# Performance work log

Measured on AMD Instinct MI355X. Metric: run time of the kernel, lower is better.

Reference implementation:

```python
import jax, jax.numpy as jnp
import numpy as np

KS = 3          # kernel_size
PAD = 1         # padding
STRIDE = 1      # stride
INC = 32
OUTC = 64
N = KS * KS     # number of sampling points


def conv2d(x, w, b, stride, pad):
    out = jax.lax.conv_general_dilated(
        x, w, (stride, stride), [(pad, pad), (pad, pad)],
        dimension_numbers=('NCHW', 'OIHW', 'NCHW'))
    return out if b is None else out + b[None, :, None, None]


def setup_inputs() -> dict:
    key = jax.random.key(0)
    k = jax.random.split(key, 5)
    x = jax.random.normal(k[0], (2, INC, 192, 192), jnp.float32)
    # main conv: kernel=ks, stride=ks, bias=None in the original
    conv_w = jax.random.normal(k[1], (OUTC, INC, KS, KS), jnp.float32) * (1.0 / np.sqrt(INC * KS * KS))
    # p_conv: weight init to 0 in the original (output = bias broadcast); unused in the math
    p_conv_w = jnp.zeros((2 * N, INC, 3, 3), jnp.float32)
    p_conv_b = jax.random.uniform(k[2], (2 * N,), jnp.float32, minval=-0.05, maxval=0.05)
    # p_conv1: produces scalar scale map A; keep it near 1 for realistic sampling
    p1_w = jax.random.normal(k[3], (1, INC, 3, 3), jnp.float32) * 0.05
    p1_b = jax.random.uniform(k[4], (1,), jnp.float32, minval=0.9, maxval=1.1)
    return {'x': x, 'conv_w': conv_w, 'p_conv_w': p_conv_w, 'p_conv_b': p_conv_b,
            'p1_w': p1_w, 'p1_b': p1_b}


def _gather_xq(xp, qx, qy, Wp):
    # xp: (b,c,Hp,Wp); qx,qy: (b,h,w,N) int -> (b,c,h,w,N)
    b, c = xp.shape[0], xp.shape[1]
    xf = xp.reshape(b, c, -1)
    idx = qx * Wp + qy  # linear index into flattened padded map (matches torch gather)
    def per_b(xf_b, idx_b):
        return xf_b[:, idx_b.ravel()].reshape((c,) + idx_b.shape)
    return jax.vmap(per_b)(xf, idx)


def _forward(x, conv_w, p_conv_w, p_conv_b, p1_w, p1_b):
    dt = x.dtype
    offset = conv2d(x, p_conv_w, p_conv_b, STRIDE, 1)   # (b,2N,h,w) -- shape-only in original
    A = conv2d(x, p1_w, p1_b, STRIDE, 1)                # (b,1,h,w) scale map
    h, w = offset.shape[2], offset.shape[3]
    xp = jnp.pad(x, ((0, 0), (0, 0), (PAD, PAD), (PAD, PAD)))
    Hp, Wp = xp.shape[2], xp.shape[3]

    # p_n: kernel-relative grid offsets, shape (1,2N,1,1)
    rng = jnp.arange(-(KS - 1) // 2, (KS - 1) // 2 + 1)
    pnx, pny = jnp.meshgrid(rng, rng, indexing='ij')
    p_n = jnp.concatenate([pnx.ravel(), pny.ravel()]).astype(dt).reshape(1, 2 * N, 1, 1)
    # p_0: absolute center coords starting at 1 (accounts for zero padding)
    gx, gy = jnp.meshgrid(jnp.arange(1, h * STRIDE + 1, STRIDE),
                          jnp.arange(1, w * STRIDE + 1, STRIDE), indexing='ij')
    p_0 = jnp.concatenate([jnp.tile(gx[None], (N, 1, 1)),
                           jnp.tile(gy[None], (N, 1, 1))], 0)[None].astype(dt)

    p = p_0 + A * p_n                       # (b,2N,h,w): scaled sampling grid
    p = jnp.transpose(p, (0, 2, 3, 1))      # (b,h,w,2N)

    q_lt = jnp.floor(p)
    q_rb = q_lt + 1
    qx_lt = jnp.clip(q_lt[..., :N], 0, Hp - 1).astype(jnp.int32)
    qy_lt = jnp.clip(q_lt[..., N:], 0, Wp - 1).astype(jnp.int32)
    qx_rb = jnp.clip(q_rb[..., :N], 0, Hp - 1).astype(jnp.int32)
    qy_rb = jnp.clip(q_rb[..., N:], 0, Wp - 1).astype(jnp.int32)

    px = jnp.clip(p[..., :N], 0, Hp - 1)
    py = jnp.clip(p[..., N:], 0, Wp - 1)

    fx_lt, fy_lt = qx_lt.astype(dt), qy_lt.astype(dt)
    fx_rb, fy_rb = qx_rb.astype(dt), qy_rb.astype(dt)
    g_lt = (1 + (fx_lt - px)) * (1 + (fy_lt - py))
    g_rb = (1 - (fx_rb - px)) * (1 - (fy_rb - py))
    g_lb = (1 + (fx_lt - px)) * (1 - (fy_rb - py))   # q_lb = (x_lt, y_rb)
    g_rt = (1 - (fx_rb - px)) * (1 + (fy_lt - py))   # q_rt = (x_rb, y_lt)

    x_lt = _gather_xq(xp, qx_lt, qy_lt, Wp)
    x_rb = _gather_xq(xp, qx_rb, qy_rb, Wp)
    x_lb = _gather_xq(xp, qx_lt, qy_rb, Wp)
    x_rt = _gather_xq(xp, qx_rb, qy_lt, Wp)

    # bilinear combine -> (b,c,h,w,N)
    x_offset = (g_lt[:, None] * x_lt + g_rb[:, None] * x_rb
                + g_lb[:, None] * x_lb + g_rt[:, None] * x_rt)

    # the ks-stride conv over the reshaped [h*ks, w*ks] map is exactly a
    # contraction over (c, n) with n = ki*ks + kj (same ordering as p_n flatten)
    wk = conv_w.reshape(conv_w.shape[0], conv_w.shape[1], N)
    out = jnp.einsum('ocn,bchwn->bohw', wk, x_offset)
    return out


def reference(x, conv_w, p_conv_w, p_conv_b, p1_w, p1_b):
    return _forward(x, conv_w, p_conv_w, p_conv_b, p1_w, p1_b)
```

## Files before the change

kernel.cpp:

```cpp
#include <hip/hip_runtime.h>

typedef __attribute__((ext_vector_type(4))) float f32x4;
typedef __attribute__((ext_vector_type(4))) int   i32x4;
typedef __attribute__((ext_vector_type(8))) short s16x8;

__device__ __forceinline__ unsigned short f2bf_rn(float f) {
  union { float f; unsigned u; } v; v.f = f;
  unsigned r = v.u + 0x7fffu + ((v.u >> 16) & 1u);
  return (unsigned short)(r >> 16);
}

__device__ __forceinline__ int packbf2(float lo, float hi) {
  union { float f; unsigned u; } a, b; a.f = lo; b.f = hi;
  return (int)__builtin_amdgcn_perm(b.u + 0x8000u, a.u + 0x8000u, 0x07060302u);
}

__device__ __forceinline__ void add8(i32x4 v, float g, f32x4& s0, f32x4& s1) {
  union { int ii; float ff; } u;
  u.ii = v[0] << 16;                  s0[0] = fmaf(g, u.ff, s0[0]);
  u.ii = v[0] & (int)0xffff0000u;     s0[1] = fmaf(g, u.ff, s0[1]);
  u.ii = v[1] << 16;                  s0[2] = fmaf(g, u.ff, s0[2]);
  u.ii = v[1] & (int)0xffff0000u;     s0[3] = fmaf(g, u.ff, s0[3]);
  u.ii = v[2] << 16;                  s1[0] = fmaf(g, u.ff, s1[0]);
  u.ii = v[2] & (int)0xffff0000u;     s1[1] = fmaf(g, u.ff, s1[1]);
  u.ii = v[3] << 16;                  s1[2] = fmaf(g, u.ff, s1[2]);
  u.ii = v[3] & (int)0xffff0000u;     s1[3] = fmaf(g, u.ff, s1[3]);
}

__device__ __forceinline__ void axis_cw(float p, int& il, int& ir, float& gl, float& gr) {
  float fl = floorf(p);
  float ql = fminf(fmaxf(fl, 0.f), 193.f);
  float qr = fminf(fmaxf(fl + 1.f, 0.f), 193.f);
  float pc = fminf(fmaxf(p, 0.f), 193.f);
  gl = 1.f + (ql - pc);
  gr = 1.f - (qr - pc);
  il = (int)ql; ir = (int)qr;
}

__global__ __launch_bounds__(256) void k_prep(const float* __restrict__ x,
                                              unsigned short* __restrict__ xp,
                                              const float* __restrict__ w,
                                              short* __restrict__ wf) {
  int t = blockIdx.x * 256 + threadIdx.x;
  if (t < 2 * 194 * 194 * 4) {
    int pix = t >> 2, c8 = t & 3;
    int b = pix / (194 * 194);
    int r = pix % (194 * 194);
    int i = r / 194 - 1, j = r % 194 - 1;
    bool ok = ((unsigned)i < 192u) && ((unsigned)j < 192u);
    const float* src = x + (size_t)b * 32 * 36864 + (size_t)(c8 * 8) * 36864 + i * 192 + j;
    unsigned v[8];
    #pragma unroll
    for (int k = 0; k < 8; k++) v[k] = ok ? (unsigned)f2bf_rn(src[k * 36864]) : 0u;
    i32x4 pv;
    pv[0] = (int)(v[0] | (v[1] << 16));
    pv[1] = (int)(v[2] | (v[3] << 16));
    pv[2] = (int)(v[4] | (v[5] << 16));
    pv[3] = (int)(v[6] | (v[7] << 16));
    *(i32x4*)(xp + (size_t)pix * 32 + c8 * 8) = pv;
  } else {
    int u = t - 2 * 194 * 194 * 4;
    if (u >= 9 * 4 * 64) return;
    int n = u / 256;
    int ot = (u / 64) % 4;
    int lane = u % 64;
    int o = ot * 16 + (lane & 15);
    int cb = (lane >> 4) * 8;
    #pragma unroll
    for (int jj = 0; jj < 8; jj++) {
      float v = w[(o * 32 + cb + jj) * 9 + n];
      wf[(size_t)u * 8 + jj] = (short)f2bf_rn(v);
    }
  }
}

__global__ __launch_bounds__(256) void k_main(const unsigned short* __restrict__ xp,
                                              const float* __restrict__ p1w,
                                              const float* __restrict__ p1b,
                                              const s16x8* __restrict__ wfv,
                                              float* __restrict__ out) {
  __shared__ float wlds[288];
  for (int idx = threadIdx.x; idx < 288; idx += 256) {
    int c = idx / 9, tap = idx % 9;
    wlds[tap * 32 + c] = p1w[idx];
  }
  __syncthreads();

  int lane = threadIdx.x & 63;
  int bs = (blockIdx.x & 7) * 144 + (blockIdx.x >> 3);
  int W = bs * 4 + (threadIdx.x >> 6);
  int b = W / 2304;
  int r = W % 2304;
  int i = r / 12;
  int j0 = (r % 12) * 16;
  int m = lane & 15, quad = lane >> 4;
  int j = j0 + m;
  const unsigned short* xpb = xp + (size_t)b * (194 * 194 * 32) + quad * 8;

  float a = 0.f;
  i32x4 vcen;
  #pragma unroll
  for (int tap = 0; tap < 9; tap++) {
    int kh = tap / 3, kw = tap % 3;
    i32x4 v = *(const i32x4*)(xpb + ((i + kh) * 194 + (j + kw)) * 32);
    if (tap == 4) vcen = v;
    const f32x4* wp = (const f32x4*)(wlds + tap * 32 + quad * 8);
    f32x4 w0 = wp[0], w1 = wp[1];
    union { int ii; float ff; } u;
    u.ii = v[0] << 16;              a = fmaf(u.ff, w0[0], a);
    u.ii = v[0] & (int)0xffff0000u; a = fmaf(u.ff, w0[1], a);
    u.ii = v[1] << 16;              a = fmaf(u.ff, w0[2], a);
    u.ii = v[1] & (int)0xffff0000u; a = fmaf(u.ff, w0[3], a);
    u.ii = v[2] << 16;              a = fmaf(u.ff, w1[0], a);
    u.ii = v[2] & (int)0xffff0000u; a = fmaf(u.ff, w1[1], a);
    u.ii = v[3] << 16;              a = fmaf(u.ff, w1[2], a);
    u.ii = v[3] & (int)0xffff0000u; a = fmaf(u.ff, w1[3], a);
  }
  a += __shfl_xor(a, 16);
  a += __shfl_xor(a, 32);
  float A = a + p1b[0];

  float cx = (float)(i + 1), cy = (float)(j + 1);
  int icx = i + 1, icy = j + 1;
  int offs[9][4];
  float gws[9][4];
  #pragma unroll
  for (int n = 0; n < 9; n++) {
    const int dx = n / 3 - 1, dy = n % 3 - 1;
    if (dx == 0 && dy == 0) continue;
    if (dy == 0) {
      int il, ir; float gl, gr;
      axis_cw(cx + A * (float)dx, il, ir, gl, gr);
      offs[n][0] = (il * 194 + icy) * 32; gws[n][0] = gl;
      offs[n][1] = (ir * 194 + icy) * 32; gws[n][1] = gr;
    } else if (dx == 0) {
      int il, ir; float gl, gr;
      axis_cw(cy + A * (float)dy, il, ir, gl, gr);
      offs[n][0] = (icx * 194 + il) * 32; gws[n][0] = gl;
      offs[n][1] = (icx * 194 + ir) * 32; gws[n][1] = gr;
    } else {
      int ilx, irx, ily, iry; float gxl, gxr, gyl, gyr;
      axis_cw(cx + A * (float)dx, ilx, irx, gxl, gxr);
      axis_cw(cy + A * (float)dy, ily, iry, gyl, gyr);
      offs[n][0] = (ilx * 194 + ily) * 32; gws[n][0] = gxl * gyl;
      offs[n][1] = (irx * 194 + iry) * 32; gws[n][1] = gxr * gyr;
      offs[n][2] = (ilx * 194 + iry) * 32; gws[n][2] = gxl * gyr;
      offs[n][3] = (irx * 194 + ily) * 32; gws[n][3] = gxr * gyl;
    }
  }

  const int cnt[9] = {4, 2, 4, 2, 0, 2, 4, 2, 4};
  i32x4 dat[9][4];
  f32x4 acc0 = {0.f, 0.f, 0.f, 0.f};
  f32x4 acc1 = acc0, acc2 = acc0, acc3 = acc0;

#define LOAD_STEP(n)                                                      \
  { _Pragma("unroll") for (int c = 0; c < 4; c++)                         \
      if (c < cnt[n]) dat[n][c] = *(const i32x4*)(xpb + offs[n][c]); }

#define PROC_STEP(n)                                                      \
  { f32x4 s0 = {0.f, 0.f, 0.f, 0.f}, s1 = s0;                             \
    _Pragma("unroll") for (int c = 0; c < 4; c++)                         \
      if (c < cnt[n]) add8(dat[n][c], gws[n][c], s0, s1);                 \
    s16x8 af; int* ai = (int*)&af;                                        \
    ai[0] = packbf2(s0[0], s0[1]); ai[1] = packbf2(s0[2], s0[3]);         \
    ai[2] = packbf2(s1[0], s1[1]); ai[3] = packbf2(s1[2], s1[3]);         \
    int wb = (n) * 256 + lane;                                            \
    acc0 = __builtin_amdgcn_mfma_f32_16x16x32_bf16(af, wfv[wb],       acc0, 0, 0, 0); \
    acc1 = __builtin_amdgcn_mfma_f32_16x16x32_bf16(af, wfv[wb + 64],  acc1, 0, 0, 0); \
    acc2 = __builtin_amdgcn_mfma_f32_16x16x32_bf16(af, wfv[wb + 128], acc2, 0, 0, 0); \
    acc3 = __builtin_amdgcn_mfma_f32_16x16x32_bf16(af, wfv[wb + 192], acc3, 0, 0, 0); }

  LOAD_STEP(0) LOAD_STEP(1) LOAD_STEP(2)
  LOAD_STEP(3) LOAD_STEP(5)
  PROC_STEP(0) PROC_STEP(1) PROC_STEP(2)
  LOAD_STEP(6) LOAD_STEP(7) LOAD_STEP(8)
  {
    s16x8 af; int* ai = (int*)&af;
    ai[0] = vcen[0]; ai[1] = vcen[1]; ai[2] = vcen[2]; ai[3] = vcen[3];
    int wb = 4 * 256 + lane;
    acc0 = __builtin_amdgcn_mfma_f32_16x16x32_bf16(af, wfv[wb],       acc0, 0, 0, 0);
    acc1 = __builtin_amdgcn_mfma_f32_16x16x32_bf16(af, wfv[wb + 64],  acc1, 0, 0, 0);
    acc2 = __builtin_amdgcn_mfma_f32_16x16x32_bf16(af, wfv[wb + 128], acc2, 0, 0, 0);
    acc3 = __builtin_amdgcn_mfma_f32_16x16x32_bf16(af, wfv[wb + 192], acc3, 0, 0, 0);
  }
  PROC_STEP(3) PROC_STEP(5)
  PROC_STEP(6) PROC_STEP(7) PROC_STEP(8)
#undef LOAD_STEP
#undef PROC_STEP

  int o0 = lane & 15;
  int jout = j0 + quad * 4;
  float* op = out + (size_t)b * 64 * 36864 + (size_t)o0 * 36864 + i * 192 + jout;
  *(f32x4*)(op) = acc0;
  *(f32x4*)(op + 16 * 36864) = acc1;
  *(f32x4*)(op + 32 * 36864) = acc2;
  *(f32x4*)(op + 48 * 36864) = acc3;
}

extern "C" void kernel_launch(void* const* d_in, const int* in_sizes, int n_in,
                              void* d_out, int out_size, void* d_ws, size_t ws_size,
                              hipStream_t stream) {
  const float* x      = (const float*)d_in[0];
  const float* conv_w = (const float*)d_in[1];
  const float* p1w    = (const float*)d_in[4];
  const float* p1b    = (const float*)d_in[5];
  float* out = (float*)d_out;

  unsigned short* xp = (unsigned short*)d_ws;
  short* wf = (short*)(xp + 2 * 194 * 194 * 32);

  int prep_threads = 2 * 194 * 194 * 4 + 9 * 4 * 64;
  k_prep<<<(prep_threads + 255) / 256, 256, 0, stream>>>(x, xp, conv_w, wf);
  k_main<<<1152, 256, 0, stream>>>(xp, p1w, p1b, (const s16x8*)wf, out);
}
```

Measured before the change: 97.83 us.

## Split output channels across two waves per segment and stream gathers per tap

Each 16-pixel segment is now handled by two waves, each computing 32 of the 64 output channels, which doubles the grid and halves the MFMA accumulators per wave. The preloaded gather buffers are replaced by per-tap load-combine-MFMA, and the scale-map dot product is split over four partial sums. Together these cut register pressure so more waves can be resident. The cost is that the scale map and all bilinear gathers are computed twice per segment, and each wave has less memory-level parallelism within itself.

```diff
diff --git a/kernel.cpp b/kernel.cpp
--- a/kernel.cpp
+++ b/kernel.cpp
@@ -87,17 +87,19 @@
   __syncthreads();
 
   int lane = threadIdx.x & 63;
-  int bs = (blockIdx.x & 7) * 144 + (blockIdx.x >> 3);
-  int W = bs * 4 + (threadIdx.x >> 6);
-  int b = W / 2304;
-  int r = W % 2304;
+  int bs = (blockIdx.x & 7) * 288 + (blockIdx.x >> 3);
+  int W2 = bs * 4 + (threadIdx.x >> 6);
+  int seg = W2 >> 1;
+  int oh  = W2 & 1;
+  int b = seg / 2304;
+  int r = seg % 2304;
   int i = r / 12;
   int j0 = (r % 12) * 16;
   int m = lane & 15, quad = lane >> 4;
   int j = j0 + m;
   const unsigned short* xpb = xp + (size_t)b * (194 * 194 * 32) + quad * 8;
 
-  float a = 0.f;
+  float a0 = 0.f, a1 = 0.f, a2 = 0.f, a3 = 0.f;
   i32x4 vcen;
   #pragma unroll
   for (int tap = 0; tap < 9; tap++) {
@@ -107,95 +109,75 @@
     const f32x4* wp = (const f32x4*)(wlds + tap * 32 + quad * 8);
     f32x4 w0 = wp[0], w1 = wp[1];
     union { int ii; float ff; } u;
-    u.ii = v[0] << 16;              a = fmaf(u.ff, w0[0], a);
-    u.ii = v[0] & (int)0xffff0000u; a = fmaf(u.ff, w0[1], a);
-    u.ii = v[1] << 16;              a = fmaf(u.ff, w0[2], a);
-    u.ii = v[1] & (int)0xffff0000u; a = fmaf(u.ff, w0[3], a);
-    u.ii = v[2] << 16;              a = fmaf(u.ff, w1[0], a);
-    u.ii = v[2] & (int)0xffff0000u; a = fmaf(u.ff, w1[1], a);
-    u.ii = v[3] << 16;              a = fmaf(u.ff, w1[2], a);
-    u.ii = v[3] & (int)0xffff0000u; a = fmaf(u.ff, w1[3], a);
+    u.ii = v[0] << 16;              a0 = fmaf(u.ff, w0[0], a0);
+    u.ii = v[0] & (int)0xffff0000u; a1 = fmaf(u.ff, w0[1], a1);
+    u.ii = v[1] << 16;              a2 = fmaf(u.ff, w0[2], a2);
+    u.ii = v[1] & (int)0xffff0000u; a3 = fmaf(u.ff, w0[3], a3);
+    u.ii = v[2] << 16;              a0 = fmaf(u.ff, w1[0], a0);
+    u.ii = v[2] & (int)0xffff0000u; a1 = fmaf(u.ff, w1[1], a1);
+    u.ii = v[3] << 16;              a2 = fmaf(u.ff, w1[2], a2);
+    u.ii = v[3] & (int)0xffff0000u; a3 = fmaf(u.ff, w1[3], a3);
   }
+  float a = (a0 + a1) + (a2 + a3);
   a += __shfl_xor(a, 16);
   a += __shfl_xor(a, 32);
   float A = a + p1b[0];
 
+  f32x4 acc0 = {0.f, 0.f, 0.f, 0.f};
+  f32x4 acc1 = acc0;
   float cx = (float)(i + 1), cy = (float)(j + 1);
   int icx = i + 1, icy = j + 1;
-  int offs[9][4];
-  float gws[9][4];
+  const int wofs = oh * 128;
+
+#define DO_MFMA(n, af)                                                            \
+  { int wb = (n) * 256 + lane + wofs;                                             \
+    acc0 = __builtin_amdgcn_mfma_f32_16x16x32_bf16(af, wfv[wb],      acc0, 0, 0, 0); \
+    acc1 = __builtin_amdgcn_mfma_f32_16x16x32_bf16(af, wfv[wb + 64], acc1, 0, 0, 0); }
+
   #pragma unroll
   for (int n = 0; n < 9; n++) {
     const int dx = n / 3 - 1, dy = n % 3 - 1;
-    if (dx == 0 && dy == 0) continue;
-    if (dy == 0) {
+    s16x8 af; int* ai = (int*)&af;
+    if (dx == 0 && dy == 0) {
+      ai[0] = vcen[0]; ai[1] = vcen[1]; ai[2] = vcen[2]; ai[3] = vcen[3];
+    } else if (dy == 0 || dx == 0) {
       int il, ir; float gl, gr;
-      axis_cw(cx + A * (float)dx, il, ir, gl, gr);
-      offs[n][0] = (il * 194 + icy) * 32; gws[n][0] = gl;
-      offs[n][1] = (ir * 194 + icy) * 32; gws[n][1] = gr;
-    } else if (dx == 0) {
-      int il, ir; float gl, gr;
-      axis_cw(cy + A * (float)dy, il, ir, gl, gr);
-      offs[n][0] = (icx * 194 + il) * 32; gws[n][0] = gl;
-      offs[n][1] = (icx * 194 + ir) * 32; gws[n][1] = gr;
+      if (dy == 0) axis_cw(cx + A * (float)dx, il, ir, gl, gr);
+      else         axis_cw(cy + A * (float)dy, il, ir, gl, gr);
+      int o_l = (dy == 0) ? (il * 194 + icy) * 32 : (icx * 194 + il) * 32;
+      int o_r = (dy == 0) ? (ir * 194 + icy) * 32 : (icx * 194 + ir) * 32;
+      i32x4 vl = *(const i32x4*)(xpb + o_l);
+      i32x4 vr = *(const i32x4*)(xpb + o_r);
+      f32x4 s0 = {0.f, 0.f, 0.f, 0.f}, s1 = s0;
+      add8(vl, gl, s0, s1);
+      add8(vr, gr, s0, s1);
+      ai[0] = packbf2(s0[0], s0[1]); ai[1] = packbf2(s0[2], s0[3]);
+      ai[2] = packbf2(s1[0], s1[1]); ai[3] = packbf2(s1[2], s1[3]);
     } else {
       int ilx, irx, ily, iry; float gxl, gxr, gyl, gyr;
       axis_cw(cx + A * (float)dx, ilx, irx, gxl, gxr);
       axis_cw(cy + A * (float)dy, ily, iry, gyl, gyr);
-      offs[n][0] = (ilx * 194 + ily) * 32; gws[n][0] = gxl * gyl;
-      offs[n][1] = (irx * 194 + iry) * 32; gws[n][1] = gxr * gyr;
-      offs[n][2] = (ilx * 194 + iry) * 32; gws[n][2] = gxl * gyr;
-      offs[n][3] = (irx * 194 + ily) * 32; gws[n][3] = gxr * gyl;
+      i32x4 vlt = *(const i32x4*)(xpb + (ilx * 194 + ily) * 32);
+      i32x4 vrb = *(const i32x4*)(xpb + (irx * 194 + iry) * 32);
+      i32x4 vlb = *(const i32x4*)(xpb + (ilx * 194 + iry) * 32);
+      i32x4 vrt = *(const i32x4*)(xpb + (irx * 194 + ily) * 32);
+      f32x4 s0 = {0.f, 0.f, 0.f, 0.f}, s1 = s0;
+      add8(vlt, gxl * gyl, s0, s1);
+      add8(vrb, gxr * gyr, s0, s1);
+      add8(vlb, gxl * gyr, s0, s1);
+      add8(vrt, gxr * gyl, s0, s1);
+      ai[0] = packbf2(s0[0], s0[1]); ai[1] = packbf2(s0[2], s0[3]);
+      ai[2] = packbf2(s1[0], s1[1]); ai[3] = packbf2(s1[2], s1[3]);
     }
+    DO_MFMA(n, af)
   }
+#undef DO_MFMA
 
-  const int cnt[9] = {4, 2, 4, 2, 0, 2, 4, 2, 4};
-  i32x4 dat[9][4];
-  f32x4 acc0 = {0.f, 0.f, 0.f, 0.f};
-  f32x4 acc1 = acc0, acc2 = acc0, acc3 = acc0;
-
-#define LOAD_STEP(n)                                                      \
-  { _Pragma("unroll") for (int c = 0; c < 4; c++)                         \
-      if (c < cnt[n]) dat[n][c] = *(const i32x4*)(xpb + offs[n][c]); }
-
-#define PROC_STEP(n)                                                      \
-  { f32x4 s0 = {0.f, 0.f, 0.f, 0.f}, s1 = s0;                             \
-    _Pragma("unroll") for (int c = 0; c < 4; c++)                         \
-      if (c < cnt[n]) add8(dat[n][c], gws[n][c], s0, s1);                 \
-    s16x8 af; int* ai = (int*)&af;                                        \
-    ai[0] = packbf2(s0[0], s0[1]); ai[1] = packbf2(s0[2], s0[3]);         \
-    ai[2] = packbf2(s1[0], s1[1]); ai[3] = packbf2(s1[2], s1[3]);         \
-    int wb = (n) * 256 + lane;                                            \
-    acc0 = __builtin_amdgcn_mfma_f32_16x16x32_bf16(af, wfv[wb],       acc0, 0, 0, 0); \
-    acc1 = __builtin_amdgcn_mfma_f32_16x16x32_bf16(af, wfv[wb + 64],  acc1, 0, 0, 0); \
-    acc2 = __builtin_amdgcn_mfma_f32_16x16x32_bf16(af, wfv[wb + 128], acc2, 0, 0, 0); \
-    acc3 = __builtin_amdgcn_mfma_f32_16x16x32_bf16(af, wfv[wb + 192], acc3, 0, 0, 0); }
-
-  LOAD_STEP(0) LOAD_STEP(1) LOAD_STEP(2)
-  LOAD_STEP(3) LOAD_STEP(5)
-  PROC_STEP(0) PROC_STEP(1) PROC_STEP(2)
-  LOAD_STEP(6) LOAD_STEP(7) LOAD_STEP(8)
-  {
-    s16x8 af; int* ai = (int*)&af;
-    ai[0] = vcen[0]; ai[1] = vcen[1]; ai[2] = vcen[2]; ai[3] = vcen[3];
-    int wb = 4 * 256 + lane;
-    acc0 = __builtin_amdgcn_mfma_f32_16x16x32_bf16(af, wfv[wb],       acc0, 0, 0, 0);
-    acc1 = __builtin_amdgcn_mfma_f32_16x16x32_bf16(af, wfv[wb + 64],  acc1, 0, 0, 0);
-    acc2 = __builtin_amdgcn_mfma_f32_16x16x32_bf16(af, wfv[wb + 128], acc2, 0, 0, 0);
-    acc3 = __builtin_amdgcn_mfma_f32_16x16x32_bf16(af, wfv[wb + 192], acc3, 0, 0, 0);
-  }
-  PROC_STEP(3) PROC_STEP(5)
-  PROC_STEP(6) PROC_STEP(7) PROC_STEP(8)
-#undef LOAD_STEP
-#undef PROC_STEP
-
-  int o0 = lane & 15;
+  int o0 = oh * 32 + (lane & 15);
   int jout = j0 + quad * 4;
   float* op = out + (size_t)b * 64 * 36864 + (size_t)o0 * 36864 + i * 192 + jout;
   *(f32x4*)(op) = acc0;
   *(f32x4*)(op + 16 * 36864) = acc1;
-  *(f32x4*)(op + 32 * 36864) = acc2;
-  *(f32x4*)(op + 48 * 36864) = acc3;
 }
 
 extern "C" void kernel_launch(void* const* d_in, const int* in_sizes, int n_in,
@@ -212,5 +194,5 @@
 
   int prep_threads = 2 * 194 * 194 * 4 + 9 * 4 * 64;
   k_prep<<<(prep_threads + 255) / 256, 256, 0, stream>>>(x, xp, conv_w, wf);
-  k_main<<<1152, 256, 0, stream>>>(xp, p1w, p1b, (const s16x8*)wf, out);
+  k_main<<<2304, 256, 0, stream>>>(xp, p1w, p1b, (const s16x8*)wf, out);
 }
```

Result: slower. 105.0 us (+7.4%).

## Move scale-map conv to prep kernel and share corner loads across taps

Applied to the files above, without the earlier changes.

The 1-channel 3x3 conv that produces the scale map A now runs in fp32 from the original input inside the prep kernel and is written to a workspace map. The main kernel just reads A. The main kernel also exploits the fact that the sampling offsets only take values cx±A and cy±A. It computes four axis weights and loads a 5x5-style grid of 25 shared corner vectors instead of 28 separate loads, and adds launch bounds for 4 blocks per SM. This cuts register pressure and redundant address math in the main kernel, at the cost of extra global traffic and work in the prep kernel.

```diff
diff --git a/kernel.cpp b/kernel.cpp
--- a/kernel.cpp
+++ b/kernel.cpp
@@ -37,12 +37,19 @@
   il = (int)ql; ir = (int)qr;
 }
 
+#define S_PAD (2 * 194 * 194 * 4)
+#define S_WF  (9 * 4 * 64)
+#define S_AM  (2 * 192 * 192 * 4)
+
 __global__ __launch_bounds__(256) void k_prep(const float* __restrict__ x,
                                               unsigned short* __restrict__ xp,
                                               const float* __restrict__ w,
-                                              short* __restrict__ wf) {
+                                              short* __restrict__ wf,
+                                              const float* __restrict__ p1w,
+                                              const float* __restrict__ p1b,
+                                              float* __restrict__ Amap) {
   int t = blockIdx.x * 256 + threadIdx.x;
-  if (t < 2 * 194 * 194 * 4) {
+  if (t < S_PAD) {
     int pix = t >> 2, c8 = t & 3;
     int b = pix / (194 * 194);
     int r = pix % (194 * 194);
@@ -58,9 +65,8 @@
     pv[2] = (int)(v[4] | (v[5] << 16));
     pv[3] = (int)(v[6] | (v[7] << 16));
     *(i32x4*)(xp + (size_t)pix * 32 + c8 * 8) = pv;
-  } else {
-    int u = t - 2 * 194 * 194 * 4;
-    if (u >= 9 * 4 * 64) return;
+  } else if (t < S_PAD + S_WF) {
+    int u = t - S_PAD;
     int n = u / 256;
     int ot = (u / 64) % 4;
     int lane = u % 64;
@@ -71,21 +77,41 @@
       float v = w[(o * 32 + cb + jj) * 9 + n];
       wf[(size_t)u * 8 + jj] = (short)f2bf_rn(v);
     }
+  } else {
+    int u = t - S_PAD - S_WF;
+    if (u >= S_AM) return;
+    int pix = u >> 2, q = u & 3;
+    int b = pix / 36864;
+    int r = pix % 36864;
+    int i = r / 192, j = r % 192;
+    const float* xb = x + (size_t)b * 32 * 36864 + (size_t)(q * 8) * 36864;
+    float a = 0.f;
+    #pragma unroll
+    for (int di = 0; di < 3; di++) {
+      int ii = i + di - 1;
+      bool rv = (unsigned)ii < 192u;
+      #pragma unroll
+      for (int dj = 0; dj < 3; dj++) {
+        int jj = j + dj - 1;
+        bool ok = rv && ((unsigned)jj < 192u);
+        int tap = di * 3 + dj;
+        #pragma unroll
+        for (int k = 0; k < 8; k++) {
+          float xv = ok ? xb[(size_t)k * 36864 + ii * 192 + jj] : 0.f;
+          a = fmaf(xv, p1w[(q * 8 + k) * 9 + tap], a);
+        }
+      }
+    }
+    a += __shfl_xor(a, 1);
+    a += __shfl_xor(a, 2);
+    if (q == 0) Amap[pix] = a + p1b[0];
   }
 }
 
-__global__ __launch_bounds__(256) void k_main(const unsigned short* __restrict__ xp,
-                                              const float* __restrict__ p1w,
-                                              const float* __restrict__ p1b,
-                                              const s16x8* __restrict__ wfv,
-                                              float* __restrict__ out) {
-  __shared__ float wlds[288];
-  for (int idx = threadIdx.x; idx < 288; idx += 256) {
-    int c = idx / 9, tap = idx % 9;
-    wlds[tap * 32 + c] = p1w[idx];
-  }
-  __syncthreads();
-
+__global__ __launch_bounds__(256, 4) void k_main(const unsigned short* __restrict__ xp,
+                                                 const float* __restrict__ Amap,
+                                                 const s16x8* __restrict__ wfv,
+                                                 float* __restrict__ out) {
   int lane = threadIdx.x & 63;
   int bs = (blockIdx.x & 7) * 144 + (blockIdx.x >> 3);
   int W = bs * 4 + (threadIdx.x >> 6);
@@ -96,98 +122,99 @@
   int m = lane & 15, quad = lane >> 4;
   int j = j0 + m;
   const unsigned short* xpb = xp + (size_t)b * (194 * 194 * 32) + quad * 8;
-
-  float a = 0.f;
-  i32x4 vcen;
-  #pragma unroll
-  for (int tap = 0; tap < 9; tap++) {
-    int kh = tap / 3, kw = tap % 3;
-    i32x4 v = *(const i32x4*)(xpb + ((i + kh) * 194 + (j + kw)) * 32);
-    if (tap == 4) vcen = v;
-    const f32x4* wp = (const f32x4*)(wlds + tap * 32 + quad * 8);
-    f32x4 w0 = wp[0], w1 = wp[1];
-    union { int ii; float ff; } u;
-    u.ii = v[0] << 16;              a = fmaf(u.ff, w0[0], a);
-    u.ii = v[0] & (int)0xffff0000u; a = fmaf(u.ff, w0[1], a);
-    u.ii = v[1] << 16;              a = fmaf(u.ff, w0[2], a);
-    u.ii = v[1] & (int)0xffff0000u; a = fmaf(u.ff, w0[3], a);
-    u.ii = v[2] << 16;              a = fmaf(u.ff, w1[0], a);
-    u.ii = v[2] & (int)0xffff0000u; a = fmaf(u.ff, w1[1], a);
-    u.ii = v[3] << 16;              a = fmaf(u.ff, w1[2], a);
-    u.ii = v[3] & (int)0xffff0000u; a = fmaf(u.ff, w1[3], a);
-  }
-  a += __shfl_xor(a, 16);
-  a += __shfl_xor(a, 32);
-  float A = a + p1b[0];
+  float A = Amap[b * 36864 + i * 192 + j];
 
   float cx = (float)(i + 1), cy = (float)(j + 1);
   int icx = i + 1, icy = j + 1;
-  int offs[9][4];
-  float gws[9][4];
-  #pragma unroll
-  for (int n = 0; n < 9; n++) {
-    const int dx = n / 3 - 1, dy = n % 3 - 1;
-    if (dx == 0 && dy == 0) continue;
-    if (dy == 0) {
-      int il, ir; float gl, gr;
-      axis_cw(cx + A * (float)dx, il, ir, gl, gr);
-      offs[n][0] = (il * 194 + icy) * 32; gws[n][0] = gl;
-      offs[n][1] = (ir * 194 + icy) * 32; gws[n][1] = gr;
-    } else if (dx == 0) {
-      int il, ir; float gl, gr;
-      axis_cw(cy + A * (float)dy, il, ir, gl, gr);
-      offs[n][0] = (icx * 194 + il) * 32; gws[n][0] = gl;
-      offs[n][1] = (icx * 194 + ir) * 32; gws[n][1] = gr;
-    } else {
-      int ilx, irx, ily, iry; float gxl, gxr, gyl, gyr;
-      axis_cw(cx + A * (float)dx, ilx, irx, gxl, gxr);
-      axis_cw(cy + A * (float)dy, ily, iry, gyl, gyr);
-      offs[n][0] = (ilx * 194 + ily) * 32; gws[n][0] = gxl * gyl;
-      offs[n][1] = (irx * 194 + iry) * 32; gws[n][1] = gxr * gyr;
-      offs[n][2] = (ilx * 194 + iry) * 32; gws[n][2] = gxl * gyr;
-      offs[n][3] = (irx * 194 + ily) * 32; gws[n][3] = gxr * gyl;
-    }
-  }
-
-  const int cnt[9] = {4, 2, 4, 2, 0, 2, 4, 2, 4};
-  i32x4 dat[9][4];
+
+  int xlm, xrm, xlp, xrp, ylm, yrm, ylp, yrp;
+  float gxlm, gxrm, gxlp, gxrp, gylm, gyrm, gylp, gyrp;
+  axis_cw(cx - A, xlm, xrm, gxlm, gxrm);
+  axis_cw(cx + A, xlp, xrp, gxlp, gxrp);
+  axis_cw(cy - A, ylm, yrm, gylm, gyrm);
+  axis_cw(cy + A, ylp, yrp, gylp, gyrp);
+
+  int rT0 = xlm * 6208, rT1 = xrm * 6208;
+  int rM  = icx * 6208;
+  int rB0 = xlp * 6208, rB1 = xrp * 6208;
+  int c0 = ylm * 32, c1 = yrm * 32, cC = icy * 32, c2 = ylp * 32, c3 = yrp * 32;
+
+  i32x4 T00 = *(const i32x4*)(xpb + rT0 + c0);
+  i32x4 T01 = *(const i32x4*)(xpb + rT0 + c1);
+  i32x4 T0C = *(const i32x4*)(xpb + rT0 + cC);
+  i32x4 T02 = *(const i32x4*)(xpb + rT0 + c2);
+  i32x4 T03 = *(const i32x4*)(xpb + rT0 + c3);
+  i32x4 T10 = *(const i32x4*)(xpb + rT1 + c0);
+  i32x4 T11 = *(const i32x4*)(xpb + rT1 + c1);
+  i32x4 T1C = *(const i32x4*)(xpb + rT1 + cC);
+  i32x4 T12 = *(const i32x4*)(xpb + rT1 + c2);
+  i32x4 T13 = *(const i32x4*)(xpb + rT1 + c3);
+  i32x4 M0 = *(const i32x4*)(xpb + rM + c0);
+  i32x4 M1 = *(const i32x4*)(xpb + rM + c1);
+  i32x4 MC = *(const i32x4*)(xpb + rM + cC);
+  i32x4 M2 = *(const i32x4*)(xpb + rM + c2);
+  i32x4 M3 = *(const i32x4*)(xpb + rM + c3);
+
   f32x4 acc0 = {0.f, 0.f, 0.f, 0.f};
   f32x4 acc1 = acc0, acc2 = acc0, acc3 = acc0;
 
-#define LOAD_STEP(n)                                                      \
-  { _Pragma("unroll") for (int c = 0; c < 4; c++)                         \
-      if (c < cnt[n]) dat[n][c] = *(const i32x4*)(xpb + offs[n][c]); }
-
-#define PROC_STEP(n)                                                      \
-  { f32x4 s0 = {0.f, 0.f, 0.f, 0.f}, s1 = s0;                             \
-    _Pragma("unroll") for (int c = 0; c < 4; c++)                         \
-      if (c < cnt[n]) add8(dat[n][c], gws[n][c], s0, s1);                 \
-    s16x8 af; int* ai = (int*)&af;                                        \
-    ai[0] = packbf2(s0[0], s0[1]); ai[1] = packbf2(s0[2], s0[3]);         \
-    ai[2] = packbf2(s1[0], s1[1]); ai[3] = packbf2(s1[2], s1[3]);         \
-    int wb = (n) * 256 + lane;                                            \
+#define MFMA4(n, af)                                                              \
+  { int wb = (n) * 256 + lane;                                                    \
     acc0 = __builtin_amdgcn_mfma_f32_16x16x32_bf16(af, wfv[wb],       acc0, 0, 0, 0); \
     acc1 = __builtin_amdgcn_mfma_f32_16x16x32_bf16(af, wfv[wb + 64],  acc1, 0, 0, 0); \
     acc2 = __builtin_amdgcn_mfma_f32_16x16x32_bf16(af, wfv[wb + 128], acc2, 0, 0, 0); \
     acc3 = __builtin_amdgcn_mfma_f32_16x16x32_bf16(af, wfv[wb + 192], acc3, 0, 0, 0); }
 
-  LOAD_STEP(0) LOAD_STEP(1) LOAD_STEP(2)
-  LOAD_STEP(3) LOAD_STEP(5)
-  PROC_STEP(0) PROC_STEP(1) PROC_STEP(2)
-  LOAD_STEP(6) LOAD_STEP(7) LOAD_STEP(8)
+#define PROC4(n, dLT, dRB, dLB, dRT, gx_l, gx_r, gy_l, gy_r)                      \
+  { f32x4 s0 = {0.f, 0.f, 0.f, 0.f}, s1 = s0;                                     \
+    add8(dLT, (gx_l) * (gy_l), s0, s1);                                           \
+    add8(dRB, (gx_r) * (gy_r), s0, s1);                                           \
+    add8(dLB, (gx_l) * (gy_r), s0, s1);                                           \
+    add8(dRT, (gx_r) * (gy_l), s0, s1);                                           \
+    s16x8 af; int* ai = (int*)&af;                                                \
+    ai[0] = packbf2(s0[0], s0[1]); ai[1] = packbf2(s0[2], s0[3]);                 \
+    ai[2] = packbf2(s1[0], s1[1]); ai[3] = packbf2(s1[2], s1[3]);                 \
+    MFMA4(n, af) }
+
+#define PROC2(n, dL, dR, g_l, g_r)                                                \
+  { f32x4 s0 = {0.f, 0.f, 0.f, 0.f}, s1 = s0;                                     \
+    add8(dL, (g_l), s0, s1);                                                      \
+    add8(dR, (g_r), s0, s1);                                                      \
+    s16x8 af; int* ai = (int*)&af;                                                \
+    ai[0] = packbf2(s0[0], s0[1]); ai[1] = packbf2(s0[2], s0[3]);                 \
+    ai[2] = packbf2(s1[0], s1[1]); ai[3] = packbf2(s1[2], s1[3]);                 \
+    MFMA4(n, af) }
+
+  PROC4(0, T00, T11, T01, T10, gxlm, gxrm, gylm, gyrm)
+  PROC2(1, T0C, T1C, gxlm, gxrm)
+  PROC4(2, T02, T13, T03, T12, gxlm, gxrm, gylp, gyrp)
+
+  i32x4 B00 = *(const i32x4*)(xpb + rB0 + c0);
+  i32x4 B01 = *(const i32x4*)(xpb + rB0 + c1);
+  i32x4 B0C = *(const i32x4*)(xpb + rB0 + cC);
+  i32x4 B02 = *(const i32x4*)(xpb + rB0 + c2);
+  i32x4 B03 = *(const i32x4*)(xpb + rB0 + c3);
+  i32x4 B10 = *(const i32x4*)(xpb + rB1 + c0);
+  i32x4 B11 = *(const i32x4*)(xpb + rB1 + c1);
+  i32x4 B1C = *(const i32x4*)(xpb + rB1 + cC);
+  i32x4 B12 = *(const i32x4*)(xpb + rB1 + c2);
+  i32x4 B13 = *(const i32x4*)(xpb + rB1 + c3);
+
+  PROC2(3, M0, M1, gylm, gyrm)
   {
     s16x8 af; int* ai = (int*)&af;
-    ai[0] = vcen[0]; ai[1] = vcen[1]; ai[2] = vcen[2]; ai[3] = vcen[3];
-    int wb = 4 * 256 + lane;
-    acc0 = __builtin_amdgcn_mfma_f32_16x16x32_bf16(af, wfv[wb],       acc0, 0, 0, 0);
-    acc1 = __builtin_amdgcn_mfma_f32_16x16x32_bf16(af, wfv[wb + 64],  acc1, 0, 0, 0);
-    acc2 = __builtin_amdgcn_mfma_f32_16x16x32_bf16(af, wfv[wb + 128], acc2, 0, 0, 0);
-    acc3 = __builtin_amdgcn_mfma_f32_16x16x32_bf16(af, wfv[wb + 192], acc3, 0, 0, 0);
+    ai[0] = MC[0]; ai[1] = MC[1]; ai[2] = MC[2]; ai[3] = MC[3];
+    MFMA4(4, af)
   }
-  PROC_STEP(3) PROC_STEP(5)
-  PROC_STEP(6) PROC_STEP(7) PROC_STEP(8)
-#undef LOAD_STEP
-#undef PROC_STEP
+  PROC2(5, M2, M3, gylp, gyrp)
+
+  PROC4(6, B00, B11, B01, B10, gxlp, gxrp, gylm, gyrm)
+  PROC2(7, B0C, B1C, gxlp, gxrp)
+  PROC4(8, B02, B13, B03, B12, gxlp, gxrp, gylp, gyrp)
+
+#undef PROC4
+#undef PROC2
+#undef MFMA4
 
   int o0 = lane & 15;
   int jout = j0 + quad * 4;
@@ -208,9 +235,10 @@
   float* out = (float*)d_out;
 
   unsigned short* xp = (unsigned short*)d_ws;
-  short* wf = (short*)(xp + 2 * 194 * 194 * 32);
-
-  int prep_threads = 2 * 194 * 194 * 4 + 9 * 4 * 64;
-  k_prep<<<(prep_threads + 255) / 256, 256, 0, stream>>>(x, xp, conv_w, wf);
-  k_main<<<1152, 256, 0, stream>>>(xp, p1w, p1b, (const s16x8*)wf, out);
-}
+  short* wf   = (short*)(xp + 2 * 194 * 194 * 32);
+  float* Amap = (float*)(wf + 9 * 256 * 8);
+
+  int prep_threads = S_PAD + S_WF + S_AM;
+  k_prep<<<(prep_threads + 255) / 256, 256, 0, stream>>>(x, xp, conv_w, wf, p1w, p1b, Amap);
+  k_main<<<1152, 256, 0, stream>>>(xp, Amap, (const s16x8*)wf, out);
+}
```

New measurement: 115.9 us. 1.18x slower.
